# Kernel tuning notes

Hardware: AMD Instinct MI355X
Metric: run time of the kernel (lower is better)

Reference implementation:

```python
import jax, jax.numpy as jnp
import numpy as np

HID = 1024
HEADS = 16
HEAD_DIM = HID // HEADS
INTER = 4 * HID
EPS = 1e-6
SCALE = 1.0 / np.sqrt(HEAD_DIM)


def setup_inputs() -> dict:
    key = jax.random.key(0)
    ks = jax.random.split(key, 8)
    s = 0.02
    return {
        "x": jax.random.normal(ks[0], (2, 2048, HID), dtype=jnp.float32),
        "wq": jax.random.normal(ks[1], (HID, HID), dtype=jnp.float32) * s,
        "wk": jax.random.normal(ks[2], (HID, HID), dtype=jnp.float32) * s,
        "wv": jax.random.normal(ks[3], (HID, HID), dtype=jnp.float32) * s,
        "wo": jax.random.normal(ks[4], (HID, HID), dtype=jnp.float32) * s,
        "w_gate": jax.random.normal(ks[5], (INTER, HID), dtype=jnp.float32) * s,
        "w_up": jax.random.normal(ks[6], (INTER, HID), dtype=jnp.float32) * s,
        "w_down": jax.random.normal(ks[7], (HID, INTER), dtype=jnp.float32) * s,
        "norm1_w": jnp.ones((HID,), dtype=jnp.float32),
        "norm2_w": jnp.ones((HID,), dtype=jnp.float32),
    }


def _rmsnorm(x, w):
    rms = jnp.sqrt(jnp.mean(x * x, axis=-1, keepdims=True) + EPS)
    return x / rms * w


def reference(x, wq, wk, wv, wo, w_gate, w_up, w_down, norm1_w, norm2_w):
    b, s, _ = x.shape
    residual = x
    h = _rmsnorm(x, norm1_w)
    # projections: nn.Linear computes h @ W.T
    q = (h @ wq.T).reshape(b, s, HEADS, HEAD_DIM).transpose(0, 2, 1, 3)
    k = (h @ wk.T).reshape(b, s, HEADS, HEAD_DIM).transpose(0, 2, 1, 3)
    v = (h @ wv.T).reshape(b, s, HEADS, HEAD_DIM).transpose(0, 2, 1, 3)
    scores = jnp.einsum("bhqd,bhkd->bhqk", q, k) * SCALE
    attn = jax.nn.softmax(scores, axis=-1)
    out = jnp.einsum("bhqk,bhkd->bhqd", attn, v)
    out = out.transpose(0, 2, 1, 3).reshape(b, s, HID)
    x = residual + out @ wo.T
    residual = x
    h = _rmsnorm(x, norm2_w)
    gate = jax.nn.silu(h @ w_gate.T)
    up = h @ w_up.T
    mlp_out = (gate * up) @ w_down.T
    return residual + mlp_out
```

## Files before the change

kernel.cpp:

```cpp
#include <hip/hip_runtime.h>
#include <hip/hip_bf16.h>

#define HID 1024
#define SEQ 2048
#define NTOK 4096
#define ATT_SCALE 0.125f

typedef __attribute__((ext_vector_type(4))) float f32x4;
typedef __attribute__((ext_vector_type(16))) float f32x16;
typedef __attribute__((ext_vector_type(8))) __bf16 bf16x8;
typedef __attribute__((ext_vector_type(4))) __bf16 bf16x4;
typedef __bf16 bf16;

__device__ __forceinline__ bf16 f2bf(float f) { return (bf16)f; }

__device__ __forceinline__ void gld_lds16(const void* g, void* l) {
  __builtin_amdgcn_global_load_lds((const __attribute__((address_space(1))) void*)g,
                                   (__attribute__((address_space(3))) void*)l,
                                   16, 0, 0);
}

__device__ __forceinline__ f32x4 mfma16(bf16x8 a, bf16x8 b, f32x4 c) {
  return __builtin_amdgcn_mfma_f32_16x16x32_bf16(a, b, c, 0, 0, 0);
}
__device__ __forceinline__ f32x16 mfma32(bf16x8 a, bf16x8 b, f32x16 c) {
  return __builtin_amdgcn_mfma_f32_32x32x16_bf16(a, b, c, 0, 0, 0);
}

struct CvtArgs {
  const float* src[7];
  bf16* dst[7];
};

__global__ __launch_bounds__(256) void cvt_weights(CvtArgs a) {
  const int g = blockIdx.x * 256 + threadIdx.x;
  const int s = g >> 18;
  const int seg = s < 4 ? s : (s < 8 ? 4 : (s < 12 ? 5 : 6));
  const int start = seg < 4 ? (seg << 18) : (((seg - 4) << 20) + (1 << 20));
  const int loc = (g - start) << 2;
  const float4 v = *(const float4*)(a.src[seg] + loc);
  bf16x4 o = {f2bf(v.x), f2bf(v.y), f2bf(v.z), f2bf(v.w)};
  *(bf16x4*)(a.dst[seg] + loc) = o;
}

__global__ __launch_bounds__(256) void rmsnorm_k(const float* __restrict__ x,
                                                 const float* __restrict__ w,
                                                 bf16* __restrict__ h) {
  const int row = blockIdx.x;
  const int tid = threadIdx.x;
  const float4 xv = *(const float4*)(x + (size_t)row * HID + tid * 4);
  float ss = xv.x * xv.x + xv.y * xv.y + xv.z * xv.z + xv.w * xv.w;
#pragma unroll
  for (int m = 1; m < 64; m <<= 1) ss += __shfl_xor(ss, m, 64);
  __shared__ float wsum[4];
  if ((tid & 63) == 0) wsum[tid >> 6] = ss;
  __syncthreads();
  const float tot = wsum[0] + wsum[1] + wsum[2] + wsum[3];
  const float inv = rsqrtf(tot * (1.0f / HID) + 1e-6f);
  const float4 wv = *(const float4*)(w + tid * 4);
  bf16x4 o = {f2bf(xv.x * inv * wv.x), f2bf(xv.y * inv * wv.y),
              f2bf(xv.z * inv * wv.z), f2bf(xv.w * inv * wv.w)};
  *(bf16x4*)(h + (size_t)row * HID + tid * 4) = o;
}

__global__ __launch_bounds__(256) void rmsnorm_red_k(const float* __restrict__ x,
                                                     const float* __restrict__ p0,
                                                     const float* __restrict__ p1,
                                                     const float* __restrict__ w,
                                                     float* __restrict__ x2,
                                                     bf16* __restrict__ h) {
  const int row = blockIdx.x;
  const int tid = threadIdx.x;
  const size_t off = (size_t)row * HID + tid * 4;
  const float4 xa = *(const float4*)(x + off);
  const float4 pa = *(const float4*)(p0 + off);
  const float4 pb = *(const float4*)(p1 + off);
  float4 xv;
  xv.x = xa.x + pa.x + pb.x;
  xv.y = xa.y + pa.y + pb.y;
  xv.z = xa.z + pa.z + pb.z;
  xv.w = xa.w + pa.w + pb.w;
  *(float4*)(x2 + off) = xv;
  float ss = xv.x * xv.x + xv.y * xv.y + xv.z * xv.z + xv.w * xv.w;
#pragma unroll
  for (int m = 1; m < 64; m <<= 1) ss += __shfl_xor(ss, m, 64);
  __shared__ float wsum[4];
  if ((tid & 63) == 0) wsum[tid >> 6] = ss;
  __syncthreads();
  const float tot = wsum[0] + wsum[1] + wsum[2] + wsum[3];
  const float inv = rsqrtf(tot * (1.0f / HID) + 1e-6f);
  const float4 wv = *(const float4*)(w + tid * 4);
  bf16x4 o = {f2bf(xv.x * inv * wv.x), f2bf(xv.y * inv * wv.y),
              f2bf(xv.z * inv * wv.z), f2bf(xv.w * inv * wv.w)};
  *(bf16x4*)(h + off) = o;
}

__global__ __launch_bounds__(256) void add3_k(float* __restrict__ out,
                                              const float* __restrict__ p0,
                                              const float* __restrict__ p1) {
  const size_t i = ((size_t)blockIdx.x * 256 + threadIdx.x) * 4;
  const float4 a = *(const float4*)(out + i);
  const float4 b = *(const float4*)(p0 + i);
  const float4 c = *(const float4*)(p1 + i);
  float4 o;
  o.x = a.x + b.x + c.x;
  o.y = a.y + b.y + c.y;
  o.z = a.z + b.z + c.z;
  o.w = a.w + b.w + c.w;
  *(float4*)(out + i) = o;
}

__global__ __launch_bounds__(512, 2) void gemm256(const bf16* __restrict__ A,
                                                  const bf16* __restrict__ B,
                                                  bf16* __restrict__ C,
                                                  int N, int K) {
  alignas(16) __shared__ bf16 As[2][256][64];
  alignas(16) __shared__ bf16 Bs[2][256][64];
  const int tid = threadIdx.x;
  const int wid = tid >> 6, lane = tid & 63;
  const int wm = wid >> 2, wn = wid & 3;
  const int bm0 = blockIdx.y << 8, bn0 = blockIdx.x << 8;

  const int srow = (wid << 3) + (lane >> 3);
  const int gch = ((lane & 7) ^ (lane >> 3)) << 3;
  const bf16* gA = A + (size_t)(bm0 + srow) * K + gch;
  const bf16* gB = B + (size_t)(bn0 + srow) * K + gch;

  const int fr = lane & 15, fc = lane >> 4, fx = lane & 7;

  f32x4 acc[8][4] = {};
  const int nt = K >> 6;

  auto stage = [&](int c, int k0) {
#pragma unroll
    for (int i = 0; i < 4; ++i)
      gld_lds16(gA + (size_t)(i * 64) * K + k0, &As[c][i * 64 + (wid << 3)][0]);
#pragma unroll
    for (int i = 0; i < 4; ++i)
      gld_lds16(gB + (size_t)(i * 64) * K + k0, &Bs[c][i * 64 + (wid << 3)][0]);
  };

  stage(0, 0);
  stage(1, 64);
  asm volatile("s_waitcnt vmcnt(8)" ::: "memory");
  __builtin_amdgcn_s_barrier();
  __builtin_amdgcn_sched_barrier(0);

  for (int t = 0; t < nt; ++t) {
    const int c = t & 1;
    bf16x8 bfrag[2][4];
#pragma unroll
    for (int s = 0; s < 2; ++s)
#pragma unroll
      for (int n = 0; n < 4; ++n)
        bfrag[s][n] = *(const bf16x8*)&Bs[c][wn * 64 + n * 16 + fr]
                                         [(((s << 2) + fc) ^ fx) << 3];
#pragma unroll
    for (int q = 0; q < 4; ++q) {
      bf16x8 af[2][2];
#pragma unroll
      for (int mi = 0; mi < 2; ++mi)
#pragma unroll
        for (int s = 0; s < 2; ++s)
          af[mi][s] = *(const bf16x8*)&As[c][wm * 128 + (q * 2 + mi) * 16 + fr]
                                           [(((s << 2) + fc) ^ fx) << 3];
      __builtin_amdgcn_s_setprio(1);
#pragma unroll
      for (int mi = 0; mi < 2; ++mi)
#pragma unroll
        for (int n = 0; n < 4; ++n)
#pragma unroll
          for (int s = 0; s < 2; ++s)
            acc[q * 2 + mi][n] = mfma16(af[mi][s], bfrag[s][n], acc[q * 2 + mi][n]);
      __builtin_amdgcn_s_setprio(0);
    }
    __builtin_amdgcn_sched_barrier(0);
    __builtin_amdgcn_s_barrier();
    __builtin_amdgcn_sched_barrier(0);
    if (t + 2 < nt) {
      stage(c, (t + 2) << 6);
      asm volatile("s_waitcnt vmcnt(8)" ::: "memory");
    } else {
      asm volatile("s_waitcnt vmcnt(0)" ::: "memory");
    }
    __builtin_amdgcn_s_barrier();
    __builtin_amdgcn_sched_barrier(0);
  }

#pragma unroll
  for (int m = 0; m < 8; ++m) {
    const int row = bm0 + wm * 128 + m * 16 + (fc << 2);
#pragma unroll
    for (int n = 0; n < 4; ++n) {
      const int col = bn0 + wn * 64 + n * 16 + fr;
#pragma unroll
      for (int r = 0; r < 4; ++r)
        C[(size_t)(row + r) * N + col] = f2bf(acc[m][n][r]);
    }
  }
}

template <int EPI>
__global__ __launch_bounds__(256) void gemm_bt(const bf16* __restrict__ A, int lda,
                                               const bf16* __restrict__ B, int ldb,
                                               void* __restrict__ C,
                                               const float* __restrict__ R,
                                               int ldc, int K) {
  alignas(16) __shared__ bf16 As[128 * 32];
  alignas(16) __shared__ bf16 Bs[128 * 32];
  const int tid = threadIdx.x;
  const int wid = tid >> 6;
  const int lane = tid & 63;
  const int bm0 = blockIdx.y * 128;
  const int bn0 = blockIdx.x * 128;
  const int wr = wid >> 1, wc = wid & 1;
  const size_t koff = (size_t)blockIdx.z * K;

  f32x4 acc[4][4] = {};

  const int sr = tid >> 2;
  const int sc = (tid & 3) << 3;
  const bf16* gA = A + (size_t)(bm0 + sr) * lda + sc + koff;
  const bf16* gB = B + (size_t)(bn0 + sr) * ldb + sc + koff;
  bf16* lA = As + wid * 512;
  bf16* lB = Bs + wid * 512;
  const int frow = lane & 15;
  const int kofs = (lane >> 4) << 3;

  for (int k0 = 0; k0 < K; k0 += 32) {
    __syncthreads();
    gld_lds16(gA + k0, lA);
    gld_lds16(gA + k0 + (size_t)64 * lda, lA + 2048);
    gld_lds16(gB + k0, lB);
    gld_lds16(gB + k0 + (size_t)64 * ldb, lB + 2048);
    __syncthreads();
    bf16x8 af[4], bfr[4];
#pragma unroll
    for (int m = 0; m < 4; ++m)
      af[m] = *(const bf16x8*)(As + (wr * 64 + m * 16 + frow) * 32 + kofs);
#pragma unroll
    for (int n = 0; n < 4; ++n)
      bfr[n] = *(const bf16x8*)(Bs + (wc * 64 + n * 16 + frow) * 32 + kofs);
#pragma unroll
    for (int m = 0; m < 4; ++m)
#pragma unroll
      for (int n = 0; n < 4; ++n)
        acc[m][n] = mfma16(af[m], bfr[n], acc[m][n]);
  }

  float* P = (EPI == 2) ? (blockIdx.z ? (float*)R : (float*)C) : nullptr;
  const int er = bm0 + wr * 64 + ((lane >> 4) << 2);
  const int ec = bn0 + wc * 64 + (lane & 15);
#pragma unroll
  for (int m = 0; m < 4; ++m)
#pragma unroll
    for (int n = 0; n < 4; ++n)
#pragma unroll
      for (int r = 0; r < 4; ++r) {
        const size_t idx = (size_t)(er + m * 16 + r) * ldc + (ec + n * 16);
        if (EPI == 0)      ((bf16*)C)[idx] = f2bf(acc[m][n][r]);
        else if (EPI == 1) ((float*)C)[idx] = R[idx] + acc[m][n][r];
        else               P[idx] = acc[m][n][r];
      }
}

__global__ __launch_bounds__(256) void vtrans_k(const bf16* __restrict__ qkv,
                                                bf16* __restrict__ vt) {
  const int bh = blockIdx.y;
  const int b = bh >> 4, head = bh & 15;
  const int st0 = blockIdx.x * 64;
  const int wid = threadIdx.x >> 6, lane = threadIdx.x & 63;
  const bf16* src = qkv + ((size_t)b * SEQ + st0 + lane) * 3072 + 2 * HID + head * 64 + wid * 16;
  bf16* dst = vt + (size_t)bh * (64 * SEQ) + st0 + lane;
#pragma unroll
  for (int half = 0; half < 2; ++half) {
    bf16x8 v = *(const bf16x8*)(src + half * 8);
#pragma unroll
    for (int i = 0; i < 8; ++i)
      dst[(size_t)(wid * 16 + half * 8 + i) * SEQ] = v[i];
  }
}

__global__ __launch_bounds__(256) void attn_k(const bf16* __restrict__ qkv,
                                              const bf16* __restrict__ vt,
                                              bf16* __restrict__ attn_out) {
  const int bh = blockIdx.y;
  const int b = bh >> 4, head = bh & 15;
  const int tid = threadIdx.x, wid = tid >> 6, lane = tid & 63;
  const int l31 = lane & 31, h = lane >> 5;
  const int r7 = l31 & 7;

  alignas(16) __shared__ bf16 Ks[64 * 64];
  alignas(16) __shared__ bf16 Vs[64 * 64];

  const float QSCALE = ATT_SCALE * 1.44269504088896f;
  const size_t tokq = (size_t)b * SEQ + blockIdx.x * 128 + wid * 32 + l31;
  bf16x8 qf[4];
#pragma unroll
  for (int s = 0; s < 4; ++s) {
    bf16x8 t = *(const bf16x8*)(qkv + tokq * 3072 + head * 64 + s * 16 + h * 8);
#pragma unroll
    for (int i = 0; i < 8; ++i) t[i] = f2bf((float)t[i] * QSCALE);
    qf[s] = t;
  }

  const int sr = tid & 63;
  const int c0 = tid >> 6;
  const int p5 = sr & 31;
  const int keyr = (sr & 32) | (p5 & 16) | (((p5 >> 2) & 1) << 3) | (((p5 >> 3) & 1) << 2) | (p5 & 3);
  const bf16* kbase = qkv + ((size_t)b * SEQ + keyr) * 3072 + HID + head * 64 + c0 * 8;
  const bf16* vbase = vt + (size_t)bh * (64 * SEQ) + (size_t)sr * SEQ + c0 * 8;
  const int w0 = sr * 64 + ((c0 ^ (sr & 7)) << 3);
  const int w1 = sr * 64 + (((c0 + 4) ^ (sr & 7)) << 3);

  bf16x8 kr0 = *(const bf16x8*)(kbase);
  bf16x8 kr1 = *(const bf16x8*)(kbase + 32);
  bf16x8 vr0 = *(const bf16x8*)(vbase);
  bf16x8 vr1 = *(const bf16x8*)(vbase + 32);

  f32x16 o0 = {}, o1 = {};
  float m = -1e30f, l = 0.f;

  for (int t0 = 0; t0 < SEQ; t0 += 64) {
    __syncthreads();
    *(bf16x8*)(Ks + w0) = kr0;
    *(bf16x8*)(Ks + w1) = kr1;
    *(bf16x8*)(Vs + w0) = vr0;
    *(bf16x8*)(Vs + w1) = vr1;
    __syncthreads();
    if (t0 + 64 < SEQ) {
      kr0 = *(const bf16x8*)(kbase + (size_t)(t0 + 64) * 3072);
      kr1 = *(const bf16x8*)(kbase + (size_t)(t0 + 64) * 3072 + 32);
      vr0 = *(const bf16x8*)(vbase + t0 + 64);
      vr1 = *(const bf16x8*)(vbase + t0 + 96);
    }

    f32x16 s0 = {}, s1 = {};
#pragma unroll
    for (int s = 0; s < 4; ++s) {
      bf16x8 k0 = *(const bf16x8*)(Ks + l31 * 64 + (((2 * s + h) ^ r7) << 3));
      s0 = mfma32(k0, qf[s], s0);
      bf16x8 k1 = *(const bf16x8*)(Ks + (32 + l31) * 64 + (((2 * s + h) ^ r7) << 3));
      s1 = mfma32(k1, qf[s], s1);
    }

    float pmax = s0[0];
#pragma unroll
    for (int i = 1; i < 16; ++i) pmax = fmaxf(pmax, s0[i]);
#pragma unroll
    for (int i = 0; i < 16; ++i) pmax = fmaxf(pmax, s1[i]);
    pmax = fmaxf(pmax, __shfl_xor(pmax, 32, 64));
    if (!__all(pmax <= m + 8.0f)) {
      const float mnew = fmaxf(m, pmax);
      const float al = exp2f(m - mnew);
      l *= al;
#pragma unroll
      for (int i = 0; i < 16; ++i) { o0[i] *= al; o1[i] *= al; }
      m = mnew;
    }

    bf16x8 pa[4];
    float sum = 0.f;
#pragma unroll
    for (int t = 0; t < 2; ++t)
#pragma unroll
      for (int j = 0; j < 8; ++j) {
        const float p = exp2f(s0[8 * t + j] - m);
        sum += p;
        pa[t][j] = f2bf(p);
      }
#pragma unroll
    for (int t = 0; t < 2; ++t)
#pragma unroll
      for (int j = 0; j < 8; ++j) {
        const float p = exp2f(s1[8 * t + j] - m);
        sum += p;
        pa[2 + t][j] = f2bf(p);
      }
    sum += __shfl_xor(sum, 32, 64);
    l += sum;

#pragma unroll
    for (int t = 0; t < 4; ++t) {
      bf16x8 v0 = *(const bf16x8*)(Vs + l31 * 64 + (((2 * t + h) ^ r7) << 3));
      o0 = mfma32(v0, pa[t], o0);
      bf16x8 v1 = *(const bf16x8*)(Vs + (32 + l31) * 64 + (((2 * t + h) ^ r7) << 3));
      o1 = mfma32(v1, pa[t], o1);
    }
  }

  const float inv = 1.0f / l;
  bf16* obase = attn_out + tokq * HID + head * 64;
#pragma unroll
  for (int rq = 0; rq < 4; ++rq) {
    bf16x4 w0v, w1v;
#pragma unroll
    for (int i = 0; i < 4; ++i) {
      w0v[i] = f2bf(o0[4 * rq + i] * inv);
      w1v[i] = f2bf(o1[4 * rq + i] * inv);
    }
    *(bf16x4*)(obase + 8 * rq + 4 * h) = w0v;
    *(bf16x4*)(obase + 32 + 8 * rq + 4 * h) = w1v;
  }
}

__global__ __launch_bounds__(256) void silu_mul_k(bf16* __restrict__ gu) {
  const int t = blockIdx.x * 256 + threadIdx.x;
  const int row = t >> 9;
  const int j = (t & 511) << 3;
  bf16* p = gu + (size_t)row * 8192 + j;
  bf16x8 g8 = *(const bf16x8*)p;
  bf16x8 u8 = *(const bf16x8*)(p + 4096);
  bf16x8 o;
#pragma unroll
  for (int i = 0; i < 8; ++i) {
    const float g = (float)g8[i], u = (float)u8[i];
    const float s = g / (1.0f + __expf(-g));
    o[i] = f2bf(s * u);
  }
  *(bf16x8*)p = o;
}

extern "C" void kernel_launch(void* const* d_in, const int* in_sizes, int n_in,
                              void* d_out, int out_size, void* d_ws, size_t ws_size,
                              hipStream_t stream) {
  const float* x  = (const float*)d_in[0];
  const float* wq = (const float*)d_in[1];
  const float* wk = (const float*)d_in[2];
  const float* wv = (const float*)d_in[3];
  const float* wo = (const float*)d_in[4];
  const float* wg = (const float*)d_in[5];
  const float* wu = (const float*)d_in[6];
  const float* wd = (const float*)d_in[7];
  const float* n1 = (const float*)d_in[8];
  const float* n2 = (const float*)d_in[9];

  char* ws = (char*)d_ws;
  bf16* wqkv_b  = (bf16*)(ws);
  bf16* wo_b    = (bf16*)(ws + 6291456);
  bf16* wgu_b   = (bf16*)(ws + 8388608);
  bf16* wd_b    = (bf16*)(ws + 25165824);
  bf16* h       = (bf16*)(ws + 33554432);
  bf16* attnout = (bf16*)(ws + 41943040);
  bf16* qkv     = (bf16*)(ws + 50331648);
  bf16* vt      = (bf16*)(ws + 75497472);
  bf16* gu      = (bf16*)(ws + 50331648);
  float* x2     = (float*)d_out;

  float* pw0 = (float*)(ws + 50331648);
  float* pw1 = (float*)(ws + 67108864);
  float* pd0 = (float*)(ws);
  float* pd1 = (float*)(ws + 33554432);

  CvtArgs ca;
  ca.src[0] = wq; ca.dst[0] = wqkv_b;
  ca.src[1] = wk; ca.dst[1] = wqkv_b + 1048576;
  ca.src[2] = wv; ca.dst[2] = wqkv_b + 2097152;
  ca.src[3] = wo; ca.dst[3] = wo_b;
  ca.src[4] = wg; ca.dst[4] = wgu_b;
  ca.src[5] = wu; ca.dst[5] = wgu_b + 4194304;
  ca.src[6] = wd; ca.dst[6] = wd_b;

  cvt_weights<<<dim3(16384), dim3(256), 0, stream>>>(ca);
  rmsnorm_k<<<dim3(NTOK), dim3(256), 0, stream>>>(x, n1, h);
  gemm256<<<dim3(12, 16), dim3(512), 0, stream>>>(h, wqkv_b, qkv, 3072, 1024);
  vtrans_k<<<dim3(32, 32), dim3(256), 0, stream>>>(qkv, vt);
  attn_k<<<dim3(16, 32), dim3(256), 0, stream>>>(qkv, vt, attnout);
  gemm_bt<2><<<dim3(8, 32, 2), dim3(256), 0, stream>>>(attnout, 1024, wo_b, 1024,
                                                       (void*)pw0, (const float*)pw1, 1024, 512);
  rmsnorm_red_k<<<dim3(NTOK), dim3(256), 0, stream>>>(x, pw0, pw1, n2, x2, h);
  gemm256<<<dim3(32, 16), dim3(512), 0, stream>>>(h, wgu_b, gu, 8192, 1024);
  silu_mul_k<<<dim3(8192), dim3(256), 0, stream>>>(gu);
  gemm_bt<2><<<dim3(8, 32, 2), dim3(256), 0, stream>>>(gu, 8192, wd_b, 4096,
                                                       (void*)pd0, (const float*)pd1, 1024, 2048);
  add3_k<<<dim3(4096), dim3(256), 0, stream>>>(x2, pd0, pd1);
}
```

Before: 441.0 us.

## Deepen gemm256 pipeline to four-stage K=32 ring with interleaved loads

Reworks the 256x256 GEMM main loop from a two-stage K=64 double buffer to a four-stage ring of K=32 slices, using a new XOR swizzle. Global-to-LDS loads for the stage three steps ahead are issued between the two halves of the MFMA work, which removes one barrier per iteration and hides load latency better. The cost is twice as many loop iterations, each with a barrier and fewer MFMAs to amortize it, plus more intricate vmcnt accounting that has to be exactly right for correctness.

After: 431.6 us. 2.1% less time.

```diff
diff --git a/kernel.cpp b/kernel.cpp
--- a/kernel.cpp
+++ b/kernel.cpp
@@ -114,75 +114,77 @@
                                                   const bf16* __restrict__ B,
                                                   bf16* __restrict__ C,
                                                   int N, int K) {
-  alignas(16) __shared__ bf16 As[2][256][64];
-  alignas(16) __shared__ bf16 Bs[2][256][64];
+  alignas(16) __shared__ bf16 As[4][256][32];
+  alignas(16) __shared__ bf16 Bs[4][256][32];
   const int tid = threadIdx.x;
   const int wid = tid >> 6, lane = tid & 63;
   const int wm = wid >> 2, wn = wid & 3;
   const int bm0 = blockIdx.y << 8, bn0 = blockIdx.x << 8;
 
-  const int srow = (wid << 3) + (lane >> 3);
-  const int gch = ((lane & 7) ^ (lane >> 3)) << 3;
-  const bf16* gA = A + (size_t)(bm0 + srow) * K + gch;
-  const bf16* gB = B + (size_t)(bn0 + srow) * K + gch;
-
-  const int fr = lane & 15, fc = lane >> 4, fx = lane & 7;
+  const int srow = (wid << 5) + (lane >> 2);
+  const int gcol = ((lane & 3) ^ ((srow >> 1) & 3)) << 3;
+  const bf16* gA = A + (size_t)(bm0 + srow) * K + gcol;
+  const bf16* gB = B + (size_t)(bn0 + srow) * K + gcol;
+
+  const int fr = lane & 15, fc = lane >> 4;
 
   f32x4 acc[8][4] = {};
-  const int nt = K >> 6;
-
-  auto stage = [&](int c, int k0) {
-#pragma unroll
-    for (int i = 0; i < 4; ++i)
-      gld_lds16(gA + (size_t)(i * 64) * K + k0, &As[c][i * 64 + (wid << 3)][0]);
-#pragma unroll
-    for (int i = 0; i < 4; ++i)
-      gld_lds16(gB + (size_t)(i * 64) * K + k0, &Bs[c][i * 64 + (wid << 3)][0]);
+  const int nt = K >> 5;
+
+  auto stageA = [&](int c, int k0) {
+    gld_lds16(gA + k0, &As[c][wid << 5][0]);
+    gld_lds16(gA + (size_t)16 * K + k0, &As[c][(wid << 5) + 16][0]);
   };
-
-  stage(0, 0);
-  stage(1, 64);
+  auto stageB = [&](int c, int k0) {
+    gld_lds16(gB + k0, &Bs[c][wid << 5][0]);
+    gld_lds16(gB + (size_t)16 * K + k0, &Bs[c][(wid << 5) + 16][0]);
+  };
+
+  stageA(0, 0);  stageB(0, 0);
+  stageA(1, 32); stageB(1, 32);
+  stageA(2, 64); stageB(2, 64);
   asm volatile("s_waitcnt vmcnt(8)" ::: "memory");
   __builtin_amdgcn_s_barrier();
   __builtin_amdgcn_sched_barrier(0);
 
   for (int t = 0; t < nt; ++t) {
-    const int c = t & 1;
-    bf16x8 bfrag[2][4];
-#pragma unroll
-    for (int s = 0; s < 2; ++s)
+    const int c = t & 3;
+    bf16x8 bfrag[4], af[4];
+#pragma unroll
+    for (int n = 0; n < 4; ++n) {
+      const int row = wn * 64 + n * 16 + fr;
+      bfrag[n] = *(const bf16x8*)&Bs[c][row][(fc ^ ((row >> 1) & 3)) << 3];
+    }
+#pragma unroll
+    for (int m = 0; m < 4; ++m) {
+      const int row = wm * 128 + m * 16 + fr;
+      af[m] = *(const bf16x8*)&As[c][row][(fc ^ ((row >> 1) & 3)) << 3];
+    }
+    if (t + 3 < nt) stageA((t + 3) & 3, (t + 3) << 5);
+    __builtin_amdgcn_s_setprio(1);
+#pragma unroll
+    for (int m = 0; m < 4; ++m)
 #pragma unroll
       for (int n = 0; n < 4; ++n)
-        bfrag[s][n] = *(const bf16x8*)&Bs[c][wn * 64 + n * 16 + fr]
-                                         [(((s << 2) + fc) ^ fx) << 3];
-#pragma unroll
-    for (int q = 0; q < 4; ++q) {
-      bf16x8 af[2][2];
-#pragma unroll
-      for (int mi = 0; mi < 2; ++mi)
-#pragma unroll
-        for (int s = 0; s < 2; ++s)
-          af[mi][s] = *(const bf16x8*)&As[c][wm * 128 + (q * 2 + mi) * 16 + fr]
-                                           [(((s << 2) + fc) ^ fx) << 3];
-      __builtin_amdgcn_s_setprio(1);
-#pragma unroll
-      for (int mi = 0; mi < 2; ++mi)
-#pragma unroll
-        for (int n = 0; n < 4; ++n)
-#pragma unroll
-          for (int s = 0; s < 2; ++s)
-            acc[q * 2 + mi][n] = mfma16(af[mi][s], bfrag[s][n], acc[q * 2 + mi][n]);
-      __builtin_amdgcn_s_setprio(0);
-    }
+        acc[m][n] = mfma16(af[m], bfrag[n], acc[m][n]);
+    __builtin_amdgcn_s_setprio(0);
+#pragma unroll
+    for (int m = 0; m < 4; ++m) {
+      const int row = wm * 128 + (m + 4) * 16 + fr;
+      af[m] = *(const bf16x8*)&As[c][row][(fc ^ ((row >> 1) & 3)) << 3];
+    }
+    if (t + 3 < nt) stageB((t + 3) & 3, (t + 3) << 5);
+    __builtin_amdgcn_s_setprio(1);
+#pragma unroll
+    for (int m = 0; m < 4; ++m)
+#pragma unroll
+      for (int n = 0; n < 4; ++n)
+        acc[m + 4][n] = mfma16(af[m], bfrag[n], acc[m + 4][n]);
+    __builtin_amdgcn_s_setprio(0);
     __builtin_amdgcn_sched_barrier(0);
-    __builtin_amdgcn_s_barrier();
-    __builtin_amdgcn_sched_barrier(0);
-    if (t + 2 < nt) {
-      stage(c, (t + 2) << 6);
-      asm volatile("s_waitcnt vmcnt(8)" ::: "memory");
-    } else {
-      asm volatile("s_waitcnt vmcnt(0)" ::: "memory");
-    }
+    if (t + 3 < nt)      asm volatile("s_waitcnt vmcnt(8)" ::: "memory");
+    else if (t + 2 < nt) asm volatile("s_waitcnt vmcnt(4)" ::: "memory");
+    else                 asm volatile("s_waitcnt vmcnt(0)" ::: "memory");
     __builtin_amdgcn_s_barrier();
     __builtin_amdgcn_sched_barrier(0);
   }
```
